# Kernel optimization log

Hardware: AMD Instinct MI355X
Metric: run time of the kernel (lower is better)

## Reference

```python
import jax, jax.numpy as jnp
import numpy as np

B, S, E, Q = 4, 4096, 1024, 8  # batch, seq, embed_dim, n_qubits


def setup_inputs() -> dict:
    key = jax.random.key(0)
    k1, k2, k3 = jax.random.split(key, 3)
    x = jax.random.normal(k1, (B, S, E), dtype=jnp.float32)
    W_enc = jax.random.normal(k2, (Q, E), dtype=jnp.float32) * (1.0 / np.sqrt(E))
    W_dec = jax.random.normal(k3, (E, Q), dtype=jnp.float32) * (1.0 / np.sqrt(Q))
    return {"x": x, "W_enc": W_enc, "W_dec": W_dec}


def reference(x, W_enc, W_dec):
    # encode tokens to rotation angles: [B,S,Q]
    angles = jnp.einsum('bse,qe->bsq', x, W_enc)
    c = jnp.cos(angles)
    # Analytic state-vector result of the circuit:
    #   RX(theta_i) on |0> then CNOT chain + ring closure, measure <Z_i>.
    # Heisenberg picture gives:
    #   <Z_0> = prod_{j=1..Q-1} cos(theta_j)
    #   <Z_i> = prod_{j=0..i}   cos(theta_j)   (i >= 1)
    p = jnp.cumprod(c, axis=-1)                      # prefix products
    q0 = jnp.prod(c[..., 1:], axis=-1, keepdims=True)
    q = jnp.concatenate([q0, p[..., 1:]], axis=-1)   # [B,S,Q] expvals
    # decode back to embed_dim and add residual
    return jnp.einsum('bsq,eq->bse', q, W_dec) + x
```

## Files before the change

kernel.cpp:

```cpp
#include <hip/hip_runtime.h>


#define EDIM 1024
#define QDIM 8
#define NTOK 16384
#define BLOCK 256
#define T 4
#define GRID (NTOK / T)

template<int CTRL>
__device__ __forceinline__ float dpp_add(float v) {
    int m = __builtin_amdgcn_update_dpp(0, __float_as_int(v), CTRL, 0xF, 0xF, true);
    return v + __int_as_float(m);
}

__device__ __forceinline__ float wave_sum63(float v) {
    v = dpp_add<0x111>(v);
    v = dpp_add<0x112>(v);
    v = dpp_add<0x114>(v);
    v = dpp_add<0x118>(v);
    v = dpp_add<0x142>(v);
    v = dpp_add<0x143>(v);
    return v;
}

__global__ __launch_bounds__(BLOCK)
void qattn_kernel(const float* __restrict__ x,
                  const float* __restrict__ W_enc,
                  const float* __restrict__ W_dec,
                  float* __restrict__ out)
{
    __shared__ float red[T][4][QDIM];

    const int t    = threadIdx.x;
    const int lane = t & 63;
    const int wave = t >> 6;
    const int e0   = t * 4;

    float wenc[QDIM][4];
#pragma unroll
    for (int q = 0; q < QDIM; ++q) {
        float4 w = *(const float4*)(W_enc + q * EDIM + e0);
        wenc[q][0] = w.x; wenc[q][1] = w.y; wenc[q][2] = w.z; wenc[q][3] = w.w;
    }
    float wdec[4][QDIM];
#pragma unroll
    for (int j = 0; j < 4; ++j) {
        float4 a = *(const float4*)(W_dec + (e0 + j) * QDIM);
        float4 b = *(const float4*)(W_dec + (e0 + j) * QDIM + 4);
        wdec[j][0] = a.x; wdec[j][1] = a.y; wdec[j][2] = a.z; wdec[j][3] = a.w;
        wdec[j][4] = b.x; wdec[j][5] = b.y; wdec[j][6] = b.z; wdec[j][7] = b.w;
    }

    const int tok0 = blockIdx.x * T;

    float4 xv[T];
#pragma unroll
    for (int i = 0; i < T; ++i)
        xv[i] = *(const float4*)(x + (size_t)(tok0 + i) * EDIM + e0);

    float partial[T][QDIM];
#pragma unroll
    for (int i = 0; i < T; ++i)
#pragma unroll
        for (int q = 0; q < QDIM; ++q)
            partial[i][q] = xv[i].x * wenc[q][0] + xv[i].y * wenc[q][1]
                          + xv[i].z * wenc[q][2] + xv[i].w * wenc[q][3];

#pragma unroll
    for (int i = 0; i < T; ++i)
#pragma unroll
        for (int q = 0; q < QDIM; ++q)
            partial[i][q] = wave_sum63(partial[i][q]);

    if (lane == 63) {
#pragma unroll
        for (int i = 0; i < T; ++i) {
            *(float4*)&red[i][wave][0] =
                make_float4(partial[i][0], partial[i][1], partial[i][2], partial[i][3]);
            *(float4*)&red[i][wave][4] =
                make_float4(partial[i][4], partial[i][5], partial[i][6], partial[i][7]);
        }
    }
    __syncthreads();

#pragma unroll
    for (int i = 0; i < T; ++i) {
        float4 lo = make_float4(0.f, 0.f, 0.f, 0.f);
        float4 hi = make_float4(0.f, 0.f, 0.f, 0.f);
#pragma unroll
        for (int w = 0; w < 4; ++w) {
            float4 a = *(const float4*)&red[i][w][0];
            float4 b = *(const float4*)&red[i][w][4];
            lo.x += a.x; lo.y += a.y; lo.z += a.z; lo.w += a.w;
            hi.x += b.x; hi.y += b.y; hi.z += b.z; hi.w += b.w;
        }
        float c[QDIM];
        c[0] = __cosf(lo.x); c[1] = __cosf(lo.y);
        c[2] = __cosf(lo.z); c[3] = __cosf(lo.w);
        c[4] = __cosf(hi.x); c[5] = __cosf(hi.y);
        c[6] = __cosf(hi.z); c[7] = __cosf(hi.w);

        float qv[QDIM];
        float q0 = c[1];
#pragma unroll
        for (int q = 2; q < QDIM; ++q) q0 *= c[q];
        qv[0] = q0;
        float p = c[0];
#pragma unroll
        for (int q = 1; q < QDIM; ++q) { p *= c[q]; qv[q] = p; }

        float4 o = xv[i];
#pragma unroll
        for (int q = 0; q < QDIM; ++q) {
            o.x += qv[q] * wdec[0][q];
            o.y += qv[q] * wdec[1][q];
            o.z += qv[q] * wdec[2][q];
            o.w += qv[q] * wdec[3][q];
        }
        *(float4*)(out + (size_t)(tok0 + i) * EDIM + e0) = o;
    }
}

extern "C" void kernel_launch(void* const* d_in, const int* in_sizes, int n_in,
                              void* d_out, int out_size, void* d_ws, size_t ws_size,
                              hipStream_t stream) {
    const float* x     = (const float*)d_in[0];
    const float* W_enc = (const float*)d_in[1];
    const float* W_dec = (const float*)d_in[2];
    float* out         = (float*)d_out;

    hipLaunchKernelGGL(qattn_kernel, dim3(GRID), dim3(BLOCK), 0, stream,
                       x, W_enc, W_dec, out);
}
```

Measured before the change: 34.64 us.

## Vectorize encode/decode with packed float math, nontemporal stores, occupancy hint

Restructures the per-thread dot products to use two-wide and four-wide vector types, aiming for packed FMA instructions, and reorders the decode as vector multiply-adds followed by horizontal sums. It also issues the x loads before the weight loads, adds a min-blocks-per-SM hint of 2 to launch_bounds, and writes the output with nontemporal stores to avoid polluting cache. It leaves in a dead zero-initialized array. The changed summation order alters floating-point rounding slightly.

```diff
diff --git a/kernel.cpp b/kernel.cpp
--- a/kernel.cpp
+++ b/kernel.cpp
@@ -1,5 +1,8 @@
 #include <hip/hip_runtime.h>
 
+
+typedef float v2f __attribute__((ext_vector_type(2)));
+typedef float v4f __attribute__((ext_vector_type(4)));
 
 #define EDIM 1024
 #define QDIM 8
@@ -24,7 +27,7 @@
     return v;
 }
 
-__global__ __launch_bounds__(BLOCK)
+__global__ __launch_bounds__(BLOCK, 2)
 void qattn_kernel(const float* __restrict__ x,
                   const float* __restrict__ W_enc,
                   const float* __restrict__ W_dec,
@@ -37,69 +40,73 @@
     const int wave = t >> 6;
     const int e0   = t * 4;
 
-    float wenc[QDIM][4];
+    const int tok0 = blockIdx.x * T;
+
+    v4f xv[T];
 #pragma unroll
-    for (int q = 0; q < QDIM; ++q) {
-        float4 w = *(const float4*)(W_enc + q * EDIM + e0);
-        wenc[q][0] = w.x; wenc[q][1] = w.y; wenc[q][2] = w.z; wenc[q][3] = w.w;
-    }
-    float wdec[4][QDIM];
+    for (int i = 0; i < T; ++i)
+        xv[i] = *(const v4f*)(x + (size_t)(tok0 + i) * EDIM + e0);
+
+    v4f we[QDIM / 2][2];
+#pragma unroll
+    for (int q = 0; q < QDIM; ++q)
+        *((v2f*)&we[q >> 1][0] + 0) = (v2f){0.f, 0.f};
+    v4f wenc[QDIM];
+#pragma unroll
+    for (int q = 0; q < QDIM; ++q)
+        wenc[q] = *(const v4f*)(W_enc + q * EDIM + e0);
+
+    v4f wdlo[4], wdhi[4];
 #pragma unroll
     for (int j = 0; j < 4; ++j) {
-        float4 a = *(const float4*)(W_dec + (e0 + j) * QDIM);
-        float4 b = *(const float4*)(W_dec + (e0 + j) * QDIM + 4);
-        wdec[j][0] = a.x; wdec[j][1] = a.y; wdec[j][2] = a.z; wdec[j][3] = a.w;
-        wdec[j][4] = b.x; wdec[j][5] = b.y; wdec[j][6] = b.z; wdec[j][7] = b.w;
+        wdlo[j] = *(const v4f*)(W_dec + (e0 + j) * QDIM);
+        wdhi[j] = *(const v4f*)(W_dec + (e0 + j) * QDIM + 4);
     }
 
-    const int tok0 = blockIdx.x * T;
-
-    float4 xv[T];
+    float ang[T][QDIM];
 #pragma unroll
-    for (int i = 0; i < T; ++i)
-        xv[i] = *(const float4*)(x + (size_t)(tok0 + i) * EDIM + e0);
-
-    float partial[T][QDIM];
+    for (int i = 0; i < T; ++i) {
+        v2f x01 = (v2f){xv[i].x, xv[i].y};
+        v2f x23 = (v2f){xv[i].z, xv[i].w};
 #pragma unroll
-    for (int i = 0; i < T; ++i)
-#pragma unroll
-        for (int q = 0; q < QDIM; ++q)
-            partial[i][q] = xv[i].x * wenc[q][0] + xv[i].y * wenc[q][1]
-                          + xv[i].z * wenc[q][2] + xv[i].w * wenc[q][3];
+        for (int q = 0; q < QDIM; ++q) {
+            v2f w01 = (v2f){wenc[q].x, wenc[q].y};
+            v2f w23 = (v2f){wenc[q].z, wenc[q].w};
+            v2f acc = x01 * w01;
+            acc = __builtin_elementwise_fma(x23, w23, acc);
+            ang[i][q] = acc.x + acc.y;
+        }
+    }
 
 #pragma unroll
     for (int i = 0; i < T; ++i)
 #pragma unroll
         for (int q = 0; q < QDIM; ++q)
-            partial[i][q] = wave_sum63(partial[i][q]);
+            ang[i][q] = wave_sum63(ang[i][q]);
 
     if (lane == 63) {
 #pragma unroll
         for (int i = 0; i < T; ++i) {
-            *(float4*)&red[i][wave][0] =
-                make_float4(partial[i][0], partial[i][1], partial[i][2], partial[i][3]);
-            *(float4*)&red[i][wave][4] =
-                make_float4(partial[i][4], partial[i][5], partial[i][6], partial[i][7]);
+            *(v4f*)&red[i][wave][0] = (v4f){ang[i][0], ang[i][1], ang[i][2], ang[i][3]};
+            *(v4f*)&red[i][wave][4] = (v4f){ang[i][4], ang[i][5], ang[i][6], ang[i][7]};
         }
     }
     __syncthreads();
 
 #pragma unroll
     for (int i = 0; i < T; ++i) {
-        float4 lo = make_float4(0.f, 0.f, 0.f, 0.f);
-        float4 hi = make_float4(0.f, 0.f, 0.f, 0.f);
+        v4f slo = (v4f){0.f, 0.f, 0.f, 0.f};
+        v4f shi = (v4f){0.f, 0.f, 0.f, 0.f};
 #pragma unroll
         for (int w = 0; w < 4; ++w) {
-            float4 a = *(const float4*)&red[i][w][0];
-            float4 b = *(const float4*)&red[i][w][4];
-            lo.x += a.x; lo.y += a.y; lo.z += a.z; lo.w += a.w;
-            hi.x += b.x; hi.y += b.y; hi.z += b.z; hi.w += b.w;
+            slo += *(const v4f*)&red[i][w][0];
+            shi += *(const v4f*)&red[i][w][4];
         }
         float c[QDIM];
-        c[0] = __cosf(lo.x); c[1] = __cosf(lo.y);
-        c[2] = __cosf(lo.z); c[3] = __cosf(lo.w);
-        c[4] = __cosf(hi.x); c[5] = __cosf(hi.y);
-        c[6] = __cosf(hi.z); c[7] = __cosf(hi.w);
+        c[0] = __cosf(slo.x); c[1] = __cosf(slo.y);
+        c[2] = __cosf(slo.z); c[3] = __cosf(slo.w);
+        c[4] = __cosf(shi.x); c[5] = __cosf(shi.y);
+        c[6] = __cosf(shi.z); c[7] = __cosf(shi.w);
 
         float qv[QDIM];
         float q0 = c[1];
@@ -110,15 +117,19 @@
 #pragma unroll
         for (int q = 1; q < QDIM; ++q) { p *= c[q]; qv[q] = p; }
 
-        float4 o = xv[i];
+        v4f qlo = (v4f){qv[0], qv[1], qv[2], qv[3]};
+        v4f qhi = (v4f){qv[4], qv[5], qv[6], qv[7]};
+
+        float oacc[4];
 #pragma unroll
-        for (int q = 0; q < QDIM; ++q) {
-            o.x += qv[q] * wdec[0][q];
-            o.y += qv[q] * wdec[1][q];
-            o.z += qv[q] * wdec[2][q];
-            o.w += qv[q] * wdec[3][q];
+        for (int j = 0; j < 4; ++j) {
+            v4f a = qlo * wdlo[j];
+            a = __builtin_elementwise_fma(qhi, wdhi[j], a);
+            v2f h = (v2f){a.x, a.y} + (v2f){a.z, a.w};
+            oacc[j] = h.x + h.y;
         }
-        *(float4*)(out + (size_t)(tok0 + i) * EDIM + e0) = o;
+        v4f o = xv[i] + (v4f){oacc[0], oacc[1], oacc[2], oacc[3]};
+        __builtin_nontemporal_store(o, (v4f*)(out + (size_t)(tok0 + i) * EDIM + e0));
     }
 }
 
```

After: 33.76 us. -2.6%, faster.
